# Performance work log

Hardware: AMD Instinct MI355X
Metric: run time of the kernel (lower is better)

## Reference

```python
import jax, jax.numpy as jnp
import numpy as np

B, T, D = 2, 2048, 2048
H = 8
KEY_DIM, VAL_DIM = 1024, 2048   # expand_k=0.5, expand_v=1.0
HK, HV = KEY_DIM // H, VAL_DIM // H
LOW_RANK = 16
GATE_NORM = 16.0
CHUNK = 64
HIDDEN = (D * 4 * 2 // 3 + 63) // 64 * 64  # 5504, exactly as GLUFFN.__init__
EPS = 1e-6


def rmsnorm(x, w):
    return x * jax.lax.rsqrt(jnp.mean(x * x, axis=-1, keepdims=True) + EPS) * w


def setup_inputs() -> dict:
    key = jax.random.key(0)
    ks = jax.random.split(key, 12)
    w = lambda k, s: jax.random.normal(k, s, jnp.float32) * 0.02
    return {
        "x": jax.random.normal(ks[0], (B, T, D), jnp.float32),
        "norm1_w": jnp.ones((D,), jnp.float32),
        "wq": w(ks[1], (D, KEY_DIM)),
        "wk": w(ks[2], (D, KEY_DIM)),
        "wv": w(ks[3], (D, VAL_DIM)),
        "gk_w1": w(ks[4], (D, LOW_RANK)),
        "gk_w2": w(ks[5], (LOW_RANK, KEY_DIM)),
        "gk_b": jnp.zeros((KEY_DIM,), jnp.float32),
        "wg": w(ks[6], (D, VAL_DIM)),
        "gnorm_w": jnp.ones((HV,), jnp.float32),
        "wo": w(ks[7], (VAL_DIM, D)),
        "ffn_norm_w": jnp.ones((D,), jnp.float32),
        "w_gate": w(ks[8], (D, HIDDEN)),
        "w_up": w(ks[9], (D, HIDDEN)),
        "w_down": w(ks[10], (HIDDEN, D)),
    }


def _gla(h, wq, wk, wv, gk_w1, gk_w2, gk_b, wg, gnorm_w, wo):
    # Gated linear attention, chunk-parallel form (fla-style):
    #   S_t = diag(exp(g_t)) S_{t-1} + k_t^T v_t ;  o_t = q_t S_t
    Bb, Tt, _ = h.shape
    nc = Tt // CHUNK

    def split(t, hd):  # [B,T,H*hd] -> [nc,B,H,CHUNK,hd]
        t = t.reshape(Bb, nc, CHUNK, H, hd)
        return jnp.transpose(t, (1, 0, 3, 2, 4))

    q = split(h @ wq, HK) * (HK ** -0.5)
    k = split(h @ wk, HK)
    v = split(h @ wv, HV)
    # low-rank forget gate, log-sigmoid scaled by gate_logit_normalizer=16
    g = split(jax.nn.log_sigmoid(h @ gk_w1 @ gk_w2 + gk_b) / GATE_NORM, HK)

    mask = jnp.tril(jnp.ones((CHUNK, CHUNK), jnp.float32))

    def step(S, inp):
        qc, kc, vc, gc = inp                       # [B,H,C,*]
        b = jnp.cumsum(gc, axis=-2)                # cumulative log-decay within chunk
        qe = qc * jnp.exp(b)
        A = jnp.einsum('bhik,bhjk->bhij', qe, kc * jnp.exp(-b)) * mask
        o = jnp.einsum('bhck,bhkv->bhcv', qe, S) + jnp.einsum('bhij,bhjv->bhiv', A, vc)
        bl = b[:, :, -1:, :]                       # decay to end of chunk
        S = jnp.exp(bl[:, :, 0, :])[..., None] * S + \
            jnp.einsum('bhck,bhcv->bhkv', kc * jnp.exp(bl - b), vc)
        return S, o

    S0 = jnp.zeros((Bb, H, HK, HV), h.dtype)
    _, o = jax.lax.scan(step, S0, (q, k, v, g))    # o: [nc,B,H,C,HV]
    o = jnp.transpose(o, (1, 0, 3, 2, 4)).reshape(Bb, Tt, H, HV)

    gate = (h @ wg).reshape(Bb, Tt, H, HV)
    # per-head RMSNorm + swish output gate (FusedRMSNormSwishGate)
    o = rmsnorm(o, gnorm_w) * gate * jax.nn.sigmoid(gate)
    return o.reshape(Bb, Tt, VAL_DIM) @ wo


def reference(x, norm1_w, wq, wk, wv, gk_w1, gk_w2, gk_b, wg, gnorm_w, wo,
              ffn_norm_w, w_gate, w_up, w_down):
    h = rmsnorm(x, norm1_w)
    x = x + _gla(h, wq, wk, wv, gk_w1, gk_w2, gk_b, wg, gnorm_w, wo)
    h2 = rmsnorm(x, ffn_norm_w)
    ffn = (jax.nn.silu(h2 @ w_gate) * (h2 @ w_up)) @ w_down  # GLUFFN, dropout=eval
    return x + ffn
```

## Files before the change

### kernel.cpp

```cpp
#include <hip/hip_runtime.h>

typedef unsigned short u16;
typedef __attribute__((ext_vector_type(8))) short bh8;
typedef __attribute__((ext_vector_type(4))) float f4;

__device__ __forceinline__ float bf2f(u16 u) {
  union { unsigned int i; float f; } x; x.i = ((unsigned int)u) << 16; return x.f;
}
__device__ __forceinline__ u16 f2bf(float f) {
  union { float f; unsigned int i; } x; x.f = f;
  unsigned int r = x.i + 0x7fffu + ((x.i >> 16) & 1u);
  return (u16)(r >> 16);
}
__device__ __forceinline__ f4 mfma16(bh8 a, bh8 b, f4 c) {
  return __builtin_amdgcn_mfma_f32_16x16x32_bf16(a, b, c, 0, 0, 0);
}
__device__ __forceinline__ void gload16(const void* g, void* l) {
  __builtin_amdgcn_global_load_lds(
      (const __attribute__((address_space(1))) void*)g,
      (__attribute__((address_space(3))) void*)l, 16, 0, 0);
}

__device__ __forceinline__ bh8 rd8(const u16* arr, int row, int col, int rowbytes) {
  return *(const bh8*)((const char*)arr + row * rowbytes + ((col * 2) ^ ((row & 7) << 4)));
}

__global__ __launch_bounds__(256)
void wtrans_k(const float* __restrict__ src, u16* __restrict__ dst, int R, int C,
              int rmul, int roff) {
  __shared__ float tile[32][33];
  int tx = threadIdx.x & 31, ty = threadIdx.x >> 5;
  int c0 = blockIdx.x * 32, r0 = blockIdx.y * 32;
#pragma unroll
  for (int yy = 0; yy < 32; yy += 8)
    tile[ty + yy][tx] = src[(size_t)(r0 + ty + yy) * C + c0 + tx];
  __syncthreads();
#pragma unroll
  for (int yy = 0; yy < 32; yy += 8)
    dst[(size_t)((c0 + ty + yy) * rmul + roff) * R + r0 + tx] = f2bf(tile[tx][ty + yy]);
}

__global__ __launch_bounds__(256)
void rmsnorm_k(const float* __restrict__ x, const float* __restrict__ w,
               u16* __restrict__ out) {
  int row = blockIdx.x, t = threadIdx.x;
  const float* xr = x + (size_t)row * 2048;
  float4 a = ((const float4*)xr)[t * 2];
  float4 b = ((const float4*)xr)[t * 2 + 1];
  float ss = a.x*a.x + a.y*a.y + a.z*a.z + a.w*a.w
           + b.x*b.x + b.y*b.y + b.z*b.z + b.w*b.w;
#pragma unroll
  for (int s = 32; s > 0; s >>= 1) ss += __shfl_xor(ss, s, 64);
  __shared__ float red[4];
  if ((t & 63) == 0) red[t >> 6] = ss;
  __syncthreads();
  float rr = rsqrtf((red[0] + red[1] + red[2] + red[3]) * (1.0f / 2048.0f) + 1e-6f);
  float v[8] = {a.x, a.y, a.z, a.w, b.x, b.y, b.z, b.w};
  int c0 = t * 8;
  u16* orow = out + (size_t)row * 2048 + c0;
#pragma unroll
  for (int j = 0; j < 8; ++j) orow[j] = f2bf(v[j] * rr * w[c0 + j]);
}

template <int EPI, typename OutT>
__global__ __launch_bounds__(256, 2)
void gemm2(const u16* __restrict__ A, const u16* __restrict__ Bt,
           OutT* __restrict__ C, void* __restrict__ aux, float scale,
           int M, int N, int K, int gx) {
  __shared__ char lds[73728];
  int t = threadIdx.x, lane = t & 63, w = t >> 6;
  int c_ = lane & 15, r_ = lane >> 4;

  int nwg = gridDim.x;
  int wg = (blockIdx.x & 7) * (nwg >> 3) + (blockIdx.x >> 3);
  int gy = nwg / gx;
  int bx = wg / gy, by = wg % gy;
  int m0 = by * 128, n0 = bx * 256;

  const size_t ldA = K, ldB = K;

  auto stageA = [&](int kt, int slot, int h) {
    int p = h * 256 + t;
    int cc = p ^ ((p >> 3) & 7);
    int m = cc >> 2, kb = cc & 3;
    const char* src = (const char*)A + ((size_t)(m0 + m) * ldA + kt * 32) * 2 + kb * 16;
    char* dst = lds + slot * 24576 + h * 4096 + w * 1024;
    gload16(src, dst);
  };
  auto stageB = [&](int kt, int slot, int qq, int j) {
    int p = qq * 512 + j * 256 + t;
    int cc = p ^ ((p >> 3) & 7);
    int n = cc >> 2, kb = cc & 3;
    const char* src = (const char*)Bt + ((size_t)(n0 + n) * ldB + kt * 32) * 2 + kb * 16;
    char* dst = lds + slot * 24576 + 8192 + (qq * 8192 + j * 4096) + w * 1024;
    gload16(src, dst);
  };
  auto rdA = [&](int slot, int mb) -> bh8 {
    int cc = (mb * 16 + c_) * 4 + r_;
    int p = cc ^ ((cc >> 3) & 7);
    return *(const bh8*)(lds + slot * 24576 + p * 16);
  };
  auto rdB = [&](int slot, int nb) -> bh8 {
    int cc = (w * 64 + nb * 16 + c_) * 4 + r_;
    int p = cc ^ ((cc >> 3) & 7);
    return *(const bh8*)(lds + slot * 24576 + 8192 + p * 16);
  };

  f4 z4 = {0.f, 0.f, 0.f, 0.f};
  f4 acc[8][4];
#pragma unroll
  for (int mb = 0; mb < 8; ++mb)
#pragma unroll
    for (int nb = 0; nb < 4; ++nb) acc[mb][nb] = z4;

  int NT = K >> 5;
  stageA(0, 0, 0); stageB(0, 0, 0, 0); stageB(0, 0, 0, 1);
  stageA(0, 0, 1); stageB(0, 0, 1, 0); stageB(0, 0, 1, 1);
  stageA(1, 1, 0); stageB(1, 1, 0, 0); stageB(1, 1, 0, 1);
  stageA(1, 1, 1); stageB(1, 1, 1, 0); stageB(1, 1, 1, 1);
  asm volatile("s_waitcnt vmcnt(6)" ::: "memory");
  __builtin_amdgcn_s_barrier();
  asm volatile("" ::: "memory");

  int slot = 0;
  for (int kt = 0; kt < NT; ++kt) {
    int fslot = slot + 2; if (fslot >= 3) fslot -= 3;
    int kts = kt + 2; if (kts >= NT) kts -= NT;
    bh8 bfr[4], afr[4];
#pragma unroll
    for (int nb = 0; nb < 4; ++nb) bfr[nb] = rdB(slot, nb);
#pragma unroll
    for (int mb = 0; mb < 4; ++mb) afr[mb] = rdA(slot, mb);
    stageA(kts, fslot, 0); stageB(kts, fslot, 0, 0); stageB(kts, fslot, 0, 1);
    __builtin_amdgcn_s_barrier();
    asm volatile("s_waitcnt lgkmcnt(0)" ::: "memory");
    __builtin_amdgcn_sched_barrier(0);
    __builtin_amdgcn_s_setprio(1);
#pragma unroll
    for (int mb = 0; mb < 4; ++mb)
#pragma unroll
      for (int nb = 0; nb < 4; ++nb) acc[mb][nb] = mfma16(afr[mb], bfr[nb], acc[mb][nb]);
    __builtin_amdgcn_s_setprio(0);
    __builtin_amdgcn_sched_barrier(0);
    __builtin_amdgcn_s_barrier();
    asm volatile("" ::: "memory");
#pragma unroll
    for (int mb = 0; mb < 4; ++mb) afr[mb] = rdA(slot, mb + 4);
    stageA(kts, fslot, 1); stageB(kts, fslot, 1, 0); stageB(kts, fslot, 1, 1);
    asm volatile("s_waitcnt vmcnt(6)" ::: "memory");
    __builtin_amdgcn_s_barrier();
    asm volatile("s_waitcnt lgkmcnt(0)" ::: "memory");
    __builtin_amdgcn_sched_barrier(0);
    __builtin_amdgcn_s_setprio(1);
#pragma unroll
    for (int mb = 0; mb < 4; ++mb)
#pragma unroll
      for (int nb = 0; nb < 4; ++nb) acc[mb + 4][nb] = mfma16(afr[mb], bfr[nb], acc[mb + 4][nb]);
    __builtin_amdgcn_s_setprio(0);
    __builtin_amdgcn_sched_barrier(0);
    __builtin_amdgcn_s_barrier();
    asm volatile("" ::: "memory");
    slot = (slot + 1 == 3) ? 0 : slot + 1;
  }
  asm volatile("s_waitcnt vmcnt(0)" ::: "memory");

#pragma unroll
  for (int mb = 0; mb < 8; ++mb) {
#pragma unroll
    for (int rr = 0; rr < 4; ++rr) {
      int row = m0 + mb * 16 + r_ * 4 + rr;
#pragma unroll
      for (int nb = 0; nb < 4; ++nb) {
        int col = n0 + w * 64 + nb * 16 + c_;
        float val = acc[mb][nb][rr];
        if (EPI == 1) {
          ((float*)C)[(size_t)row * N + col] = val + ((const float*)aux)[(size_t)row * N + col];
        } else if (EPI == 5) {
          if (col < 1024) ((u16*)C)[(size_t)row * 1024 + col] = f2bf(val * scale);
          else ((u16*)aux)[(size_t)row * 1024 + col - 1024] = f2bf(val);
        } else if (EPI == 4) {
          if (col < 2048) {
            int bb = row >> 11, t2 = row & 2047;
            int pan = ((bb << 5) + (t2 >> 6)) * 8 + (col >> 8);
            int ii = t2 & 63, vv = col & 255;
            *(u16*)((char*)C + (size_t)pan * 32768 + vv * 128 + ((ii * 2) ^ ((vv & 7) << 4)))
                = f2bf(val);
          } else {
            ((u16*)aux)[(size_t)row * 2048 + col - 2048] = f2bf(val);
          }
        } else if (EPI == 6) {
          float other = __shfl_xor(val, 1, 64);
          if (lane & 1) {
            float gv = other;
            ((u16*)C)[(size_t)row * 5504 + (col >> 1)] = f2bf(val * (gv / (1.f + expf(-gv))));
          }
        }
      }
    }
  }
}

__global__ __launch_bounds__(256)
void lowrank_k(const u16* __restrict__ h, const float* __restrict__ w1,
               const float* __restrict__ w2, const float* __restrict__ bias,
               float* __restrict__ g) {
  int row = blockIdx.x, t = threadIdx.x, lane = t & 63, wave = t >> 6;
  const u16* hr = h + (size_t)row * 2048;
  bh8 hv = *(const bh8*)&hr[t * 8];
  float p[16];
#pragma unroll
  for (int j = 0; j < 16; ++j) p[j] = 0.f;
#pragma unroll
  for (int kk = 0; kk < 8; ++kk) {
    float f = bf2f((u16)hv[kk]);
    const float* wrow = w1 + (size_t)(t * 8 + kk) * 16;
#pragma unroll
    for (int j = 0; j < 16; ++j) p[j] += f * wrow[j];
  }
#pragma unroll
  for (int j = 0; j < 16; ++j)
#pragma unroll
    for (int s = 32; s > 0; s >>= 1) p[j] += __shfl_xor(p[j], s, 64);
  __shared__ float gl[4][16];
  if (lane == 0) {
#pragma unroll
    for (int j = 0; j < 16; ++j) gl[wave][j] = p[j];
  }
  __syncthreads();
  float glow[16];
#pragma unroll
  for (int j = 0; j < 16; ++j) glow[j] = gl[0][j] + gl[1][j] + gl[2][j] + gl[3][j];
  float* grow = g + (size_t)row * 1024;
#pragma unroll
  for (int nn = 0; nn < 4; ++nn) {
    int n = nn * 256 + t;
    float z = bias[n];
#pragma unroll
    for (int j = 0; j < 16; ++j) z += glow[j] * w2[j * 1024 + n];
    float ls = fminf(z, 0.f) - log1pf(expf(-fabsf(z)));
    grow[n] = ls * (1.0f / 16.0f);
  }
}

__global__ __launch_bounds__(128)
void gprep_k(u16* __restrict__ q, u16* __restrict__ k, const float* __restrict__ g,
             u16* __restrict__ keT, float* __restrict__ ebl) {
  int bid = blockIdx.x;
  int h = bid & 7, bc = bid >> 3;
  int b = bc >> 5, c = bc & 31;
  int ch = threadIdx.x;
  size_t base = ((size_t)(b * 2048 + c * 64)) * 1024 + h * 128 + ch;
  char* keTp = (char*)keT + (size_t)bid * 16384 + ch * 128;
  int sw = (ch & 7) << 4;
  float bacc = 0.f;
  for (int i8 = 0; i8 < 8; ++i8) {
    u16 kp[8];
#pragma unroll
    for (int e = 0; e < 8; ++e) {
      size_t off = base + (size_t)(i8 * 8 + e) * 1024;
      bacc += g[off];
      float eb = __expf(bacc);
      float reb = __builtin_amdgcn_rcpf(eb);
      float qv = bf2f(q[off]), kv = bf2f(k[off]);
      q[off] = f2bf(qv * eb);
      u16 kev = f2bf(kv * reb);
      k[off] = kev;
      kp[e] = kev;
    }
    *(bh8*)(keTp + ((i8 * 16) ^ sw)) = *(const bh8*)kp;
  }
  ebl[(size_t)bid * 128 + ch] = __expf(bacc);
}

__global__ __launch_bounds__(256)
void gla_scan(const u16* __restrict__ qg, const u16* __restrict__ kg,
              const u16* __restrict__ keTg, const u16* __restrict__ vTg,
              const float* __restrict__ eblg, float* __restrict__ outp) {
  __shared__ u16 qeL[64 * 128];
  __shared__ u16 keL[64 * 128];
  __shared__ u16 kTL[128 * 64];
  __shared__ u16 vTL[64 * 64];
  __shared__ u16 AL[64 * 64];
  __shared__ u16 SbL[64 * 128];
  __shared__ float SfL[64][133];

  int t = threadIdx.x, lane = t & 63, w = t >> 6;
  int vb = blockIdx.x & 3, bh = blockIdx.x >> 2;
  int b = bh >> 3, h = bh & 7;
  int c_ = lane & 15, r_ = lane >> 4;
  f4 z4 = {0.f, 0.f, 0.f, 0.f};

  for (int i = t; i < 64 * 128; i += 256) SbL[i] = 0;
  for (int i = t; i < 64 * 133; i += 256) ((float*)SfL)[i] = 0.f;

  const char* qbase = (const char*)qg + (size_t)b * 2048 * 2048 + h * 256;
  const char* kbase = (const char*)kg + (size_t)b * 2048 * 2048 + h * 256;
  int rowoff = (t >> 4) * 2048 + (t & 15) * 16;
  int4 pq[4], pk[4], pkt[4], pvt[2];

#define LOADCH(cc)                                                              \
  {                                                                             \
    const char* qc = qbase + (size_t)(cc) * 64 * 2048;                          \
    const char* kc = kbase + (size_t)(cc) * 64 * 2048;                          \
    int panel_ = ((b * 32 + (cc)) * 8 + h);                                     \
    const char* ktc = (const char*)keTg + (size_t)panel_ * 16384;               \
    const char* vtc = (const char*)vTg + (size_t)panel_ * 32768 + vb * 8192;    \
    _Pragma("unroll")                                                           \
    for (int j = 0; j < 4; ++j) {                                               \
      pq[j] = *(const int4*)(qc + j * 16 * 2048 + rowoff);                      \
      pk[j] = *(const int4*)(kc + j * 16 * 2048 + rowoff);                      \
      pkt[j] = *(const int4*)(ktc + j * 4096 + t * 16);                         \
    }                                                                           \
    _Pragma("unroll")                                                           \
    for (int j = 0; j < 2; ++j) pvt[j] = *(const int4*)(vtc + j * 4096 + t * 16); \
  }

  LOADCH(0);
  for (int c = 0; c < 32; ++c) {
#pragma unroll
    for (int j = 0; j < 4; ++j) {
      int L = j * 4096 + t * 16;
      int d = (L & ~255) | ((L & 255) ^ (((L >> 8) & 7) << 4));
      *(int4*)((char*)qeL + d) = pq[j];
      *(int4*)((char*)keL + d) = pk[j];
      *(int4*)((char*)kTL + L) = pkt[j];
    }
#pragma unroll
    for (int j = 0; j < 2; ++j) *(int4*)((char*)vTL + j * 4096 + t * 16) = pvt[j];
    if (c < 31) LOADCH(c + 1);
    int panel = ((b * 32 + c) * 8 + h);
    float eblr[2][4];
#pragma unroll
    for (int kt = 0; kt < 2; ++kt)
#pragma unroll
      for (int r = 0; r < 4; ++r)
        eblr[kt][r] = eblg[(size_t)panel * 128 + w * 32 + kt * 16 + r_ * 4 + r];
    __syncthreads();

    f4 accA[4] = {z4, z4, z4, z4};
    f4 accS[2][4] = {{z4, z4, z4, z4}, {z4, z4, z4, z4}};
#pragma unroll
    for (int ks = 0; ks < 4; ++ks) {
      bh8 a = rd8(qeL, w * 16 + c_, ks * 32 + r_ * 8, 256);
#pragma unroll
      for (int n = 0; n < 4; ++n)
        accA[n] = mfma16(a, rd8(keL, n * 16 + c_, ks * 32 + r_ * 8, 256), accA[n]);
    }
#pragma unroll
    for (int ks = 0; ks < 2; ++ks) {
      bh8 bf_[4];
#pragma unroll
      for (int n = 0; n < 4; ++n) bf_[n] = rd8(vTL, n * 16 + c_, ks * 32 + r_ * 8, 128);
#pragma unroll
      for (int kt = 0; kt < 2; ++kt) {
        bh8 a = rd8(kTL, w * 32 + kt * 16 + c_, ks * 32 + r_ * 8, 128);
#pragma unroll
        for (int n = 0; n < 4; ++n) accS[kt][n] = mfma16(a, bf_[n], accS[kt][n]);
      }
    }
#pragma unroll
    for (int n = 0; n < 4; ++n)
#pragma unroll
      for (int r = 0; r < 4; ++r) {
        int i = w * 16 + r_ * 4 + r, j = n * 16 + c_;
        *(u16*)((char*)AL + i * 128 + ((j * 2) ^ ((i & 7) << 4))) =
            (j <= i) ? f2bf(accA[n][r]) : (u16)0;
      }
    __syncthreads();

    f4 acco[4] = {z4, z4, z4, z4};
#pragma unroll
    for (int ks = 0; ks < 4; ++ks) {
      bh8 a = rd8(qeL, w * 16 + c_, ks * 32 + r_ * 8, 256);
#pragma unroll
      for (int n = 0; n < 4; ++n)
        acco[n] = mfma16(a, rd8(SbL, n * 16 + c_, ks * 32 + r_ * 8, 256), acco[n]);
    }
#pragma unroll
    for (int ks = 0; ks < 2; ++ks) {
      bh8 a = rd8(AL, w * 16 + c_, ks * 32 + r_ * 8, 128);
#pragma unroll
      for (int n = 0; n < 4; ++n)
        acco[n] = mfma16(a, rd8(vTL, n * 16 + c_, ks * 32 + r_ * 8, 128), acco[n]);
    }
    {
      size_t obase = (size_t)(b * 2048 + c * 64 + w * 16 + r_ * 4) * 2048 + h * 256 + vb * 64;
#pragma unroll
      for (int n = 0; n < 4; ++n)
#pragma unroll
        for (int r = 0; r < 4; ++r)
          outp[obase + (size_t)r * 2048 + n * 16 + c_] = acco[n][r];
    }
    __syncthreads();

#pragma unroll
    for (int kt = 0; kt < 2; ++kt)
#pragma unroll
      for (int n = 0; n < 4; ++n)
#pragma unroll
        for (int r = 0; r < 4; ++r) {
          int kk = w * 32 + kt * 16 + r_ * 4 + r;
          int vcol = n * 16 + c_;
          float nv = eblr[kt][r] * (SfL[vcol][kk] + accS[kt][n][r]);
          SfL[vcol][kk] = nv;
          *(u16*)((char*)SbL + vcol * 256 + ((kk * 2) ^ ((vcol & 7) << 4))) = f2bf(nv);
        }
    __syncthreads();
  }
#undef LOADCH
}

__global__ __launch_bounds__(256)
void ogate_k(const float* __restrict__ o, const u16* __restrict__ gate,
             const float* __restrict__ gw, u16* __restrict__ og) {
  int tok = blockIdx.x, t = threadIdx.x;
  int head = t >> 5, l32 = t & 31, v0 = l32 * 8;
  size_t base = (size_t)tok * 2048 + head * 256 + v0;
  float4 a = *(const float4*)&o[base];
  float4 b = *(const float4*)&o[base + 4];
  float ov[8] = {a.x, a.y, a.z, a.w, b.x, b.y, b.z, b.w};
  float ss = 0.f;
#pragma unroll
  for (int j = 0; j < 8; ++j) ss += ov[j] * ov[j];
#pragma unroll
  for (int s = 16; s > 0; s >>= 1) ss += __shfl_xor(ss, s, 32);
  float rr = rsqrtf(ss * (1.0f / 256.0f) + 1e-6f);
#pragma unroll
  for (int j = 0; j < 8; ++j) {
    float gv = bf2f(gate[base + j]);
    float val = ov[j] * rr * gw[v0 + j];
    og[base + j] = f2bf(val * gv / (1.f + expf(-gv)));
  }
}

extern "C" void kernel_launch(void* const* d_in, const int* in_sizes, int n_in,
                              void* d_out, int out_size, void* d_ws, size_t ws_size,
                              hipStream_t stream) {
  (void)in_sizes; (void)n_in; (void)out_size; (void)ws_size;
  const float* x = (const float*)d_in[0];
  const float* n1w = (const float*)d_in[1];
  const float* wq = (const float*)d_in[2];
  const float* wk = (const float*)d_in[3];
  const float* wv = (const float*)d_in[4];
  const float* gw1 = (const float*)d_in[5];
  const float* gw2 = (const float*)d_in[6];
  const float* gb = (const float*)d_in[7];
  const float* wg = (const float*)d_in[8];
  const float* gnw = (const float*)d_in[9];
  const float* wo = (const float*)d_in[10];
  const float* fnw = (const float*)d_in[11];
  const float* wgate = (const float*)d_in[12];
  const float* wup = (const float*)d_in[13];
  const float* wdown = (const float*)d_in[14];
  float* out = (float*)d_out;

  char* ws = (char*)d_ws;
  size_t off = 0;
  auto alloc = [&](size_t bytes) { size_t p = off; off += (bytes + 255) & ~(size_t)255; return p; };
  u16* wqT = (u16*)(ws + alloc(2ull * 1024 * 2048));
  u16* wkT = (u16*)(ws + alloc(2ull * 1024 * 2048));
  u16* wvT = (u16*)(ws + alloc(2ull * 2048 * 2048));
  u16* wgT = (u16*)(ws + alloc(2ull * 2048 * 2048));
  u16* woT = (u16*)(ws + alloc(2ull * 2048 * 2048));
  u16* btGU = (u16*)(ws + alloc(2ull * 11008 * 2048));
  u16* wdT = (u16*)(ws + alloc(2ull * 2048 * 5504));
  u16* h_bf = (u16*)(ws + alloc(2ull * 4096 * 2048));
  u16* q_bf = (u16*)(ws + alloc(2ull * 4096 * 1024));
  u16* k_bf = (u16*)(ws + alloc(2ull * 4096 * 1024));
  u16* vT_g = (u16*)(ws + alloc(2ull * 4096 * 2048));
  u16* gate_bf = (u16*)(ws + alloc(2ull * 4096 * 2048));
  float* g_f = (float*)(ws + alloc(4ull * 4096 * 1024));
  float* o_f = (float*)(ws + alloc(4ull * 4096 * 2048));
  u16* mid = (u16*)(ws + alloc(2ull * 4096 * 5504));
  float* ebl_g = (float*)(ws + alloc(4ull * 512 * 128));
  u16* keT_g = h_bf;
  u16* og = h_bf;
  u16* h2 = q_bf;
  float* x2 = o_f;

  dim3 blk(256);
  wtrans_k<<<dim3(32, 64), blk, 0, stream>>>(wq, wqT, 2048, 1024, 1, 0);
  wtrans_k<<<dim3(32, 64), blk, 0, stream>>>(wk, wkT, 2048, 1024, 1, 0);
  wtrans_k<<<dim3(64, 64), blk, 0, stream>>>(wv, wvT, 2048, 2048, 1, 0);
  wtrans_k<<<dim3(64, 64), blk, 0, stream>>>(wg, wgT, 2048, 2048, 1, 0);
  wtrans_k<<<dim3(64, 64), blk, 0, stream>>>(wo, woT, 2048, 2048, 1, 0);
  wtrans_k<<<dim3(172, 64), blk, 0, stream>>>(wgate, btGU, 2048, 5504, 2, 0);
  wtrans_k<<<dim3(172, 64), blk, 0, stream>>>(wup, btGU, 2048, 5504, 2, 1);
  wtrans_k<<<dim3(64, 172), blk, 0, stream>>>(wdown, wdT, 5504, 2048, 1, 0);

  rmsnorm_k<<<4096, blk, 0, stream>>>(x, n1w, h_bf);

  gemm2<5, u16><<<256, blk, 0, stream>>>(h_bf, wqT, q_bf, k_bf, 0.08838834764831845f,
                                         4096, 2048, 2048, 8);
  gemm2<4, u16><<<512, blk, 0, stream>>>(h_bf, wvT, vT_g, gate_bf, 1.f,
                                         4096, 4096, 2048, 16);
  lowrank_k<<<4096, blk, 0, stream>>>(h_bf, gw1, gw2, gb, g_f);

  gprep_k<<<512, dim3(128), 0, stream>>>(q_bf, k_bf, g_f, keT_g, ebl_g);

  gla_scan<<<64, blk, 0, stream>>>(q_bf, k_bf, keT_g, vT_g, ebl_g, o_f);

  ogate_k<<<4096, blk, 0, stream>>>(o_f, gate_bf, gnw, og);

  gemm2<1, float><<<256, blk, 0, stream>>>(og, woT, x2, (void*)x, 1.f,
                                           4096, 2048, 2048, 8);

  rmsnorm_k<<<4096, blk, 0, stream>>>(x2, fnw, h2);

  gemm2<6, u16><<<1376, blk, 0, stream>>>(h2, btGU, mid, nullptr, 1.f,
                                          4096, 11008, 2048, 43);
  gemm2<1, float><<<256, blk, 0, stream>>>(mid, wdT, out, x2, 1.f,
                                           4096, 2048, 5504, 8);
}
```

Measured before the change: 1.081 ms.

## Add 128x128 GEMM tile variant for N=2048 GEMMs and precompute addresses

Templates the GEMM on tile width, adding a 128x128 variant with a 2x2 wave layout. The q/k, wo and down-projection GEMMs use it so they launch 512 workgroups instead of 256 and fill more of the 256 CUs. The main loop is also rewritten: global and LDS addresses are computed once up front, and the loop is unrolled over the three buffer slots as a single k-step per tile. Smaller tiles lower arithmetic intensity and raise LDS and global traffic per FLOP.

```diff
diff --git a/kernel.cpp b/kernel.cpp
--- a/kernel.cpp
+++ b/kernel.cpp
@@ -62,116 +62,121 @@
   for (int j = 0; j < 8; ++j) orow[j] = f2bf(v[j] * rr * w[c0 + j]);
 }
 
-template <int EPI, typename OutT>
+template <int EPI, int BN, typename OutT>
 __global__ __launch_bounds__(256, 2)
 void gemm2(const u16* __restrict__ A, const u16* __restrict__ Bt,
            OutT* __restrict__ C, void* __restrict__ aux, float scale,
            int M, int N, int K, int gx) {
-  __shared__ char lds[73728];
+  constexpr int SB = (BN == 256) ? 24576 : 16384;
+  constexpr int NBS = (BN == 256) ? 4 : 2;
+  constexpr int MB = (BN == 256) ? 8 : 4;
+  __shared__ char lds[3 * SB];
   int t = threadIdx.x, lane = t & 63, w = t >> 6;
   int c_ = lane & 15, r_ = lane >> 4;
+  int wm = (BN == 256) ? 0 : (w >> 1);
+  int wn = (BN == 256) ? w : (w & 1);
 
   int nwg = gridDim.x;
   int wg = (blockIdx.x & 7) * (nwg >> 3) + (blockIdx.x >> 3);
   int gy = nwg / gx;
   int bx = wg / gy, by = wg % gy;
-  int m0 = by * 128, n0 = bx * 256;
-
-  const size_t ldA = K, ldB = K;
-
-  auto stageA = [&](int kt, int slot, int h) {
+  int m0 = by * 128, n0 = bx * BN;
+
+  const char* baseA[2];
+#pragma unroll
+  for (int h = 0; h < 2; ++h) {
     int p = h * 256 + t;
     int cc = p ^ ((p >> 3) & 7);
-    int m = cc >> 2, kb = cc & 3;
-    const char* src = (const char*)A + ((size_t)(m0 + m) * ldA + kt * 32) * 2 + kb * 16;
-    char* dst = lds + slot * 24576 + h * 4096 + w * 1024;
-    gload16(src, dst);
-  };
-  auto stageB = [&](int kt, int slot, int qq, int j) {
-    int p = qq * 512 + j * 256 + t;
+    baseA[h] = (const char*)A + ((size_t)(m0 + (cc >> 2)) * K + (cc & 3) * 8) * 2;
+  }
+  const char* baseB[NBS];
+#pragma unroll
+  for (int s = 0; s < NBS; ++s) {
+    int p = s * 256 + t;
     int cc = p ^ ((p >> 3) & 7);
-    int n = cc >> 2, kb = cc & 3;
-    const char* src = (const char*)Bt + ((size_t)(n0 + n) * ldB + kt * 32) * 2 + kb * 16;
-    char* dst = lds + slot * 24576 + 8192 + (qq * 8192 + j * 4096) + w * 1024;
-    gload16(src, dst);
-  };
-  auto rdA = [&](int slot, int mb) -> bh8 {
-    int cc = (mb * 16 + c_) * 4 + r_;
-    int p = cc ^ ((cc >> 3) & 7);
-    return *(const bh8*)(lds + slot * 24576 + p * 16);
-  };
-  auto rdB = [&](int slot, int nb) -> bh8 {
-    int cc = (w * 64 + nb * 16 + c_) * 4 + r_;
-    int p = cc ^ ((cc >> 3) & 7);
-    return *(const bh8*)(lds + slot * 24576 + 8192 + p * 16);
-  };
+    baseB[s] = (const char*)Bt + ((size_t)(n0 + (cc >> 2)) * K + (cc & 3) * 8) * 2;
+  }
+  int offA[MB], offB[4];
+#pragma unroll
+  for (int mb = 0; mb < MB; ++mb) {
+    int cc = (wm * 64 + mb * 16 + c_) * 4 + r_;
+    offA[mb] = (cc ^ ((cc >> 3) & 7)) * 16;
+  }
+#pragma unroll
+  for (int nb = 0; nb < 4; ++nb) {
+    int cc = (wn * 64 + nb * 16 + c_) * 4 + r_;
+    offB[nb] = (cc ^ ((cc >> 3) & 7)) * 16 + 8192;
+  }
+  int ldsW = w * 1024;
 
   f4 z4 = {0.f, 0.f, 0.f, 0.f};
-  f4 acc[8][4];
-#pragma unroll
-  for (int mb = 0; mb < 8; ++mb)
+  f4 acc[MB][4];
+#pragma unroll
+  for (int mb = 0; mb < MB; ++mb)
 #pragma unroll
     for (int nb = 0; nb < 4; ++nb) acc[mb][nb] = z4;
 
   int NT = K >> 5;
-  stageA(0, 0, 0); stageB(0, 0, 0, 0); stageB(0, 0, 0, 1);
-  stageA(0, 0, 1); stageB(0, 0, 1, 0); stageB(0, 0, 1, 1);
-  stageA(1, 1, 0); stageB(1, 1, 0, 0); stageB(1, 1, 0, 1);
-  stageA(1, 1, 1); stageB(1, 1, 1, 0); stageB(1, 1, 1, 1);
-  asm volatile("s_waitcnt vmcnt(6)" ::: "memory");
+
+#define STAGE(S, ko)                                                        \
+  {                                                                         \
+    _Pragma("unroll") for (int h = 0; h < 2; ++h)                           \
+        gload16(baseA[h] + (ko), lds + (S) * SB + h * 4096 + ldsW);         \
+    _Pragma("unroll") for (int s = 0; s < NBS; ++s)                         \
+        gload16(baseB[s] + (ko), lds + (S) * SB + 8192 + s * 4096 + ldsW);  \
+  }
+#define WAIT_VM()                                                           \
+  if (BN == 256) { asm volatile("s_waitcnt vmcnt(6)" ::: "memory"); }       \
+  else { asm volatile("s_waitcnt vmcnt(4)" ::: "memory"); }
+#define KTILE(S)                                                            \
+  {                                                                         \
+    bh8 afr[MB], bfr[4];                                                    \
+    _Pragma("unroll") for (int nb = 0; nb < 4; ++nb)                        \
+        bfr[nb] = *(const bh8*)(lds + (S) * SB + offB[nb]);                 \
+    _Pragma("unroll") for (int mb = 0; mb < MB; ++mb)                       \
+        afr[mb] = *(const bh8*)(lds + (S) * SB + offA[mb]);                 \
+    int kts = kt + 2; if (kts >= NT) kts -= NT;                             \
+    STAGE(((S) + 2) % 3, kts << 6);                                         \
+    WAIT_VM();                                                              \
+    __builtin_amdgcn_s_barrier();                                           \
+    asm volatile("s_waitcnt lgkmcnt(0)" ::: "memory");                      \
+    __builtin_amdgcn_sched_barrier(0);                                      \
+    __builtin_amdgcn_s_setprio(1);                                          \
+    _Pragma("unroll") for (int mb = 0; mb < MB; ++mb)                       \
+        _Pragma("unroll") for (int nb = 0; nb < 4; ++nb)                    \
+            acc[mb][nb] = mfma16(afr[mb], bfr[nb], acc[mb][nb]);            \
+    __builtin_amdgcn_s_setprio(0);                                          \
+    __builtin_amdgcn_sched_barrier(0);                                      \
+    __builtin_amdgcn_s_barrier();                                           \
+    asm volatile("" ::: "memory");                                          \
+  }
+
+  STAGE(0, 0);
+  STAGE(1, 64);
+  WAIT_VM();
   __builtin_amdgcn_s_barrier();
   asm volatile("" ::: "memory");
 
-  int slot = 0;
-  for (int kt = 0; kt < NT; ++kt) {
-    int fslot = slot + 2; if (fslot >= 3) fslot -= 3;
-    int kts = kt + 2; if (kts >= NT) kts -= NT;
-    bh8 bfr[4], afr[4];
-#pragma unroll
-    for (int nb = 0; nb < 4; ++nb) bfr[nb] = rdB(slot, nb);
-#pragma unroll
-    for (int mb = 0; mb < 4; ++mb) afr[mb] = rdA(slot, mb);
-    stageA(kts, fslot, 0); stageB(kts, fslot, 0, 0); stageB(kts, fslot, 0, 1);
-    __builtin_amdgcn_s_barrier();
-    asm volatile("s_waitcnt lgkmcnt(0)" ::: "memory");
-    __builtin_amdgcn_sched_barrier(0);
-    __builtin_amdgcn_s_setprio(1);
-#pragma unroll
-    for (int mb = 0; mb < 4; ++mb)
-#pragma unroll
-      for (int nb = 0; nb < 4; ++nb) acc[mb][nb] = mfma16(afr[mb], bfr[nb], acc[mb][nb]);
-    __builtin_amdgcn_s_setprio(0);
-    __builtin_amdgcn_sched_barrier(0);
-    __builtin_amdgcn_s_barrier();
-    asm volatile("" ::: "memory");
-#pragma unroll
-    for (int mb = 0; mb < 4; ++mb) afr[mb] = rdA(slot, mb + 4);
-    stageA(kts, fslot, 1); stageB(kts, fslot, 1, 0); stageB(kts, fslot, 1, 1);
-    asm volatile("s_waitcnt vmcnt(6)" ::: "memory");
-    __builtin_amdgcn_s_barrier();
-    asm volatile("s_waitcnt lgkmcnt(0)" ::: "memory");
-    __builtin_amdgcn_sched_barrier(0);
-    __builtin_amdgcn_s_setprio(1);
-#pragma unroll
-    for (int mb = 0; mb < 4; ++mb)
-#pragma unroll
-      for (int nb = 0; nb < 4; ++nb) acc[mb + 4][nb] = mfma16(afr[mb], bfr[nb], acc[mb + 4][nb]);
-    __builtin_amdgcn_s_setprio(0);
-    __builtin_amdgcn_sched_barrier(0);
-    __builtin_amdgcn_s_barrier();
-    asm volatile("" ::: "memory");
-    slot = (slot + 1 == 3) ? 0 : slot + 1;
+  int kt = 0;
+  while (true) {
+    KTILE(0); if (++kt == NT) break;
+    KTILE(1); if (++kt == NT) break;
+    KTILE(2); if (++kt == NT) break;
   }
   asm volatile("s_waitcnt vmcnt(0)" ::: "memory");
-
-#pragma unroll
-  for (int mb = 0; mb < 8; ++mb) {
+#undef KTILE
+#undef WAIT_VM
+#undef STAGE
+
+  int rowBase = m0 + wm * 64;
+#pragma unroll
+  for (int mb = 0; mb < MB; ++mb) {
 #pragma unroll
     for (int rr = 0; rr < 4; ++rr) {
-      int row = m0 + mb * 16 + r_ * 4 + rr;
+      int row = rowBase + mb * 16 + r_ * 4 + rr;
 #pragma unroll
       for (int nb = 0; nb < 4; ++nb) {
-        int col = n0 + w * 64 + nb * 16 + c_;
+        int col = n0 + wn * 64 + nb * 16 + c_;
         float val = acc[mb][nb][rr];
         if (EPI == 1) {
           ((float*)C)[(size_t)row * N + col] = val + ((const float*)aux)[(size_t)row * N + col];
@@ -490,10 +495,10 @@
 
   rmsnorm_k<<<4096, blk, 0, stream>>>(x, n1w, h_bf);
 
-  gemm2<5, u16><<<256, blk, 0, stream>>>(h_bf, wqT, q_bf, k_bf, 0.08838834764831845f,
-                                         4096, 2048, 2048, 8);
-  gemm2<4, u16><<<512, blk, 0, stream>>>(h_bf, wvT, vT_g, gate_bf, 1.f,
-                                         4096, 4096, 2048, 16);
+  gemm2<5, 128, u16><<<512, blk, 0, stream>>>(h_bf, wqT, q_bf, k_bf, 0.08838834764831845f,
+                                              4096, 2048, 2048, 16);
+  gemm2<4, 256, u16><<<512, blk, 0, stream>>>(h_bf, wvT, vT_g, gate_bf, 1.f,
+                                              4096, 4096, 2048, 16);
   lowrank_k<<<4096, blk, 0, stream>>>(h_bf, gw1, gw2, gb, g_f);
 
   gprep_k<<<512, dim3(128), 0, stream>>>(q_bf, k_bf, g_f, keT_g, ebl_g);
@@ -502,13 +507,13 @@
 
   ogate_k<<<4096, blk, 0, stream>>>(o_f, gate_bf, gnw, og);
 
-  gemm2<1, float><<<256, blk, 0, stream>>>(og, woT, x2, (void*)x, 1.f,
-                                           4096, 2048, 2048, 8);
+  gemm2<1, 128, float><<<512, blk, 0, stream>>>(og, woT, x2, (void*)x, 1.f,
+                                                4096, 2048, 2048, 16);
 
   rmsnorm_k<<<4096, blk, 0, stream>>>(x2, fnw, h2);
 
-  gemm2<6, u16><<<1376, blk, 0, stream>>>(h2, btGU, mid, nullptr, 1.f,
-                                          4096, 11008, 2048, 43);
-  gemm2<1, float><<<256, blk, 0, stream>>>(mid, wdT, out, x2, 1.f,
-                                           4096, 2048, 5504, 8);
-}
+  gemm2<6, 256, u16><<<1376, blk, 0, stream>>>(h2, btGU, mid, nullptr, 1.f,
+                                               4096, 11008, 2048, 43);
+  gemm2<1, 128, float><<<512, blk, 0, stream>>>(mid, wdT, out, x2, 1.f,
+                                                4096, 2048, 5504, 16);
+}
```

New measurement: 1.017 ms. 1.06x faster.
